# Optimization experiments

Hardware: AMD Instinct MI355X
Metric: run time of the kernel (lower is better)

Reference implementation:

```python
import jax, jax.numpy as jnp
import numpy as np


def setup_inputs() -> dict:
    key = jax.random.key(0)
    k1, k2 = jax.random.split(key)
    B, F, E = 16384, 200, 64
    features = jax.random.normal(k1, (B, F), dtype=jnp.float32)
    # per-feature Linear(1, E, bias=False) weights, stacked: [F, E]
    W = jax.random.uniform(k2, (F, E), dtype=jnp.float32, minval=-1e-4, maxval=1e-4)
    return {"features": features, "W": W}


def reference(features, W):
    # emb[b, f, e] = features[b, f] * W[f, e]  (rank-1 'Linear(1,E)' per feature)
    # sum over features then square:  (sum_f f_bf * W_fe)^2 = (features @ W)^2
    sum_emb = jnp.einsum('bf,fe->be', features, W)            # [B, E]
    # sum over features of squares: sum_f (f_bf * W_fe)^2 = (features^2) @ (W^2)
    sq_sum = jnp.einsum('bf,fe->be', features * features, W * W)  # [B, E]
    # FM second-order term, summed over embedding dim, keepdim
    predicts = jnp.sum(sum_emb * sum_emb - sq_sum, axis=1, keepdims=True)  # [B, 1]
    return predicts
```

## Files before the change

### kernel.cpp

```cpp
#include <hip/hip_runtime.h>


constexpr int F   = 200;
constexpr int E   = 64;
constexpr int WAVES = 4;
constexpr int RPW   = 8;
constexpr int RPB   = WAVES * RPW;

__global__ __launch_bounds__(256)
void fm_kernel(const float* __restrict__ X, const float* __restrict__ W,
               float* __restrict__ out, int nrows)
{
    __shared__ float wlds[F * E];
    __shared__ float slds[F];

    const int tid = threadIdx.x;

    for (int idx = tid; idx < F * E; idx += 256)
        wlds[idx] = W[idx];
    __syncthreads();

    for (int f = tid; f < F; f += 256) {
        float a = 0.f;
        #pragma unroll
        for (int k = 0; k < E; ++k) {
            int e = (k + f) & (E - 1);
            float w = wlds[f * E + e];
            a = fmaf(w, w, a);
        }
        slds[f] = a;
    }
    __syncthreads();

    const int lane = tid & 63;
    const int wave = __builtin_amdgcn_readfirstlane((int)(tid >> 6));
    const int rowBase = (int)blockIdx.x * RPB + wave * RPW;
    const float* __restrict__ xb = X + (size_t)rowBase * F;

    float q[RPW];
    #pragma unroll
    for (int r = 0; r < RPW; ++r) q[r] = 0.f;
    for (int f = lane; f < F; f += 64) {
        float s = slds[f];
        #pragma unroll
        for (int r = 0; r < RPW; ++r) {
            float x = xb[(size_t)r * F + f];
            q[r] = fmaf(x * x, s, q[r]);
        }
    }

    float acc[RPW];
    #pragma unroll
    for (int r = 0; r < RPW; ++r) acc[r] = 0.f;

    for (int f0 = 0; f0 < F; f0 += 4) {
        float w0 = wlds[(f0 + 0) * E + lane];
        float w1 = wlds[(f0 + 1) * E + lane];
        float w2 = wlds[(f0 + 2) * E + lane];
        float w3 = wlds[(f0 + 3) * E + lane];
        #pragma unroll
        for (int r = 0; r < RPW; ++r) {
            const float* xp = xb + (size_t)r * F + f0;
            float x0 = xp[0], x1 = xp[1], x2 = xp[2], x3 = xp[3];
            acc[r] = fmaf(x0, w0, acc[r]);
            acc[r] = fmaf(x1, w1, acc[r]);
            acc[r] = fmaf(x2, w2, acc[r]);
            acc[r] = fmaf(x3, w3, acc[r]);
        }
    }

    #pragma unroll
    for (int r = 0; r < RPW; ++r) {
        float v = fmaf(acc[r], acc[r], -q[r]);
        #pragma unroll
        for (int off = 32; off > 0; off >>= 1)
            v += __shfl_xor(v, off, 64);
        if (lane == 0 && rowBase + r < nrows)
            out[rowBase + r] = v;
    }
}

extern "C" void kernel_launch(void* const* d_in, const int* in_sizes, int n_in,
                              void* d_out, int out_size, void* d_ws, size_t ws_size,
                              hipStream_t stream) {
    const float* X = (const float*)d_in[0];
    const float* W = (const float*)d_in[1];
    float* out = (float*)d_out;

    const int B = in_sizes[0] / F;
    const int grid = (B + RPB - 1) / RPB;
    fm_kernel<<<grid, 256, 0, stream>>>(X, W, out, B);
}
```

Measured before the change: 77.98 us.

## Compute sum embedding with fp16 MFMA and fused sq-sum reduction

Replaces the scalar fp32 FMA matmul with fp16 MFMA 16x16x32 on a K-padded LDS tile. Weights are scaled by a constant before fp16 conversion to avoid underflow, and the result is rescaled afterward. W is loaded and converted with vectorized float4 reads, with per-feature squared norms computed by shuffles, and the square-sum term is computed while staging X into LDS. This trades fp32 precision for matrix-core throughput and removes the tail bound check, so B must be a multiple of 32.

```diff
diff --git a/kernel.cpp b/kernel.cpp
--- a/kernel.cpp
+++ b/kernel.cpp
@@ -1,83 +1,118 @@
 #include <hip/hip_runtime.h>
 
 
-constexpr int F   = 200;
-constexpr int E   = 64;
-constexpr int WAVES = 4;
-constexpr int RPW   = 8;
-constexpr int RPB   = WAVES * RPW;
+constexpr int F  = 200;
+constexpr int RB = 32;
+constexpr int KP = 232;
+constexpr float WSCALE = 8192.0f;
+constexpr float OSCALE = 1.0f / (WSCALE * WSCALE);
+
+typedef _Float16 half8 __attribute__((ext_vector_type(8)));
+typedef _Float16 half4 __attribute__((ext_vector_type(4)));
+typedef float floatx4 __attribute__((ext_vector_type(4)));
 
 __global__ __launch_bounds__(256)
-void fm_kernel(const float* __restrict__ X, const float* __restrict__ W,
-               float* __restrict__ out, int nrows)
+void fm_mfma(const float* __restrict__ X, const float* __restrict__ W,
+             float* __restrict__ out)
 {
-    __shared__ float wlds[F * E];
-    __shared__ float slds[F];
+    __shared__ alignas(16) _Float16 xt[RB][KP];
+    __shared__ alignas(16) _Float16 wt[64][KP];
+    __shared__ alignas(16) float    sf[F];
+    __shared__ alignas(16) float    res[RB];
 
-    const int tid = threadIdx.x;
+    const int t    = threadIdx.x;
+    const int lane = t & 63;
 
-    for (int idx = tid; idx < F * E; idx += 256)
-        wlds[idx] = W[idx];
-    __syncthreads();
-
-    for (int f = tid; f < F; f += 256) {
-        float a = 0.f;
-        #pragma unroll
-        for (int k = 0; k < E; ++k) {
-            int e = (k + f) & (E - 1);
-            float w = wlds[f * E + e];
-            a = fmaf(w, w, a);
+    {
+        const floatx4* W4 = (const floatx4*)W;
+        for (int j = 0; j < 13; ++j) {
+            int i = t + 256 * j;
+            if (i < 3200) {
+                floatx4 w4 = W4[i];
+                int f  = i >> 4;
+                int e0 = (i & 15) * 4;
+                float ss = w4.x*w4.x + w4.y*w4.y + w4.z*w4.z + w4.w*w4.w;
+                ss += __shfl_xor(ss, 1, 64);
+                ss += __shfl_xor(ss, 2, 64);
+                ss += __shfl_xor(ss, 4, 64);
+                ss += __shfl_xor(ss, 8, 64);
+                if ((t & 15) == 0) sf[f] = ss;
+                wt[e0 + 0][f] = (_Float16)(w4.x * WSCALE);
+                wt[e0 + 1][f] = (_Float16)(w4.y * WSCALE);
+                wt[e0 + 2][f] = (_Float16)(w4.z * WSCALE);
+                wt[e0 + 3][f] = (_Float16)(w4.w * WSCALE);
+            }
         }
-        slds[f] = a;
+        half8 z = {};
+        *(half8*)&wt[t >> 2][200 + 8 * (t & 3)] = z;
+        if (t < 128) *(half8*)&xt[t >> 2][200 + 8 * (t & 3)] = z;
     }
     __syncthreads();
 
-    const int lane = tid & 63;
-    const int wave = __builtin_amdgcn_readfirstlane((int)(tid >> 6));
-    const int rowBase = (int)blockIdx.x * RPB + wave * RPW;
-    const float* __restrict__ xb = X + (size_t)rowBase * F;
+    const int rowBase = (int)blockIdx.x * RB;
+    {
+        int r = t >> 3, sub = t & 7;
+        const floatx4* Xr = (const floatx4*)(X + (size_t)(rowBase + r) * F);
+        float q = 0.f;
+        for (int j = 0; j < 7; ++j) {
+            int f4 = sub + 8 * j;
+            if (f4 < 50) {
+                floatx4 x4 = Xr[f4];
+                floatx4 s4 = *(const floatx4*)&sf[4 * f4];
+                q += x4.x*x4.x*s4.x + x4.y*x4.y*s4.y + x4.z*x4.z*s4.z + x4.w*x4.w*s4.w;
+                half4 h;
+                h[0] = (_Float16)x4.x; h[1] = (_Float16)x4.y;
+                h[2] = (_Float16)x4.z; h[3] = (_Float16)x4.w;
+                *(half4*)&xt[r][4 * f4] = h;
+            }
+        }
+        q += __shfl_xor(q, 1, 64);
+        q += __shfl_xor(q, 2, 64);
+        q += __shfl_xor(q, 4, 64);
+        if (sub == 0) res[r] = -q;
+    }
+    __syncthreads();
 
-    float q[RPW];
-    #pragma unroll
-    for (int r = 0; r < RPW; ++r) q[r] = 0.f;
-    for (int f = lane; f < F; f += 64) {
-        float s = slds[f];
+    {
+        const int w  = t >> 6;
+        const int mt = (w & 1) * 16;
+        const int nb = (w >> 1) * 32;
+        const int lm = lane & 15, lq = lane >> 4;
+
+        const half8* ap  = (const half8*)&xt[mt + lm][lq * 8];
+        const half8* b0p = (const half8*)&wt[nb + lm][lq * 8];
+        const half8* b1p = (const half8*)&wt[nb + 16 + lm][lq * 8];
+
+        floatx4 acc0 = {}, acc1 = {};
         #pragma unroll
-        for (int r = 0; r < RPW; ++r) {
-            float x = xb[(size_t)r * F + f];
-            q[r] = fmaf(x * x, s, q[r]);
+        for (int kk = 0; kk < 7; ++kk) {
+            half8 a  = ap [kk * 4];
+            half8 b0 = b0p[kk * 4];
+            half8 b1 = b1p[kk * 4];
+            acc0 = __builtin_amdgcn_mfma_f32_16x16x32_f16(a, b0, acc0, 0, 0, 0);
+            acc1 = __builtin_amdgcn_mfma_f32_16x16x32_f16(a, b1, acc1, 0, 0, 0);
+        }
+
+        float p[4];
+        #pragma unroll
+        for (int r2 = 0; r2 < 4; ++r2)
+            p[r2] = acc0[r2]*acc0[r2] + acc1[r2]*acc1[r2];
+        #pragma unroll
+        for (int r2 = 0; r2 < 4; ++r2) {
+            p[r2] += __shfl_xor(p[r2], 1, 64);
+            p[r2] += __shfl_xor(p[r2], 2, 64);
+            p[r2] += __shfl_xor(p[r2], 4, 64);
+            p[r2] += __shfl_xor(p[r2], 8, 64);
+        }
+        if (lm == 0) {
+            #pragma unroll
+            for (int r2 = 0; r2 < 4; ++r2)
+                atomicAdd(&res[mt + lq * 4 + r2], p[r2] * OSCALE);
         }
     }
+    __syncthreads();
 
-    float acc[RPW];
-    #pragma unroll
-    for (int r = 0; r < RPW; ++r) acc[r] = 0.f;
-
-    for (int f0 = 0; f0 < F; f0 += 4) {
-        float w0 = wlds[(f0 + 0) * E + lane];
-        float w1 = wlds[(f0 + 1) * E + lane];
-        float w2 = wlds[(f0 + 2) * E + lane];
-        float w3 = wlds[(f0 + 3) * E + lane];
-        #pragma unroll
-        for (int r = 0; r < RPW; ++r) {
-            const float* xp = xb + (size_t)r * F + f0;
-            float x0 = xp[0], x1 = xp[1], x2 = xp[2], x3 = xp[3];
-            acc[r] = fmaf(x0, w0, acc[r]);
-            acc[r] = fmaf(x1, w1, acc[r]);
-            acc[r] = fmaf(x2, w2, acc[r]);
-            acc[r] = fmaf(x3, w3, acc[r]);
-        }
-    }
-
-    #pragma unroll
-    for (int r = 0; r < RPW; ++r) {
-        float v = fmaf(acc[r], acc[r], -q[r]);
-        #pragma unroll
-        for (int off = 32; off > 0; off >>= 1)
-            v += __shfl_xor(v, off, 64);
-        if (lane == 0 && rowBase + r < nrows)
-            out[rowBase + r] = v;
-    }
+    if (t < RB) out[rowBase + t] = res[t];
 }
 
 extern "C" void kernel_launch(void* const* d_in, const int* in_sizes, int n_in,
@@ -88,6 +123,5 @@
     float* out = (float*)d_out;
 
     const int B = in_sizes[0] / F;
-    const int grid = (B + RPB - 1) / RPB;
-    fm_kernel<<<grid, 256, 0, stream>>>(X, W, out, B);
+    fm_mfma<<<B / RB, 256, 0, stream>>>(X, W, out);
 }
```

Result: faster. 67.54 us (-13.4%).
